# Kernel optimization log

Measured on AMD Instinct MI355X. Metric: run time of the kernel, lower is better.

## Reference

```python
import jax, jax.numpy as jnp
import numpy as np
import math

LOG2PI = math.log(2.0 * math.pi)
ALPHA, BETA, GAMMA = 1.0, 4.0, 1.0  # coefficients (mi, tc, dw_kl)


def gaussian_log_density(samples, mean, log_var):
    inv_sigma = jnp.exp(-log_var)
    tmp = samples - mean
    return -0.5 * (tmp * tmp * inv_sigma + log_var + LOG2PI)


def log_importance_weight_matrix(batch_size, dataset_size):
    # Faithful port of the TF/beta-tcvae MSS importance weights.
    N = float(dataset_size)
    M = batch_size - 1
    strat_weight = (N - M) / (N * M)
    W = jnp.full((batch_size, batch_size), 1.0 / M, dtype=jnp.float32)
    W = W.at[:, 0].set(1.0 / N)
    W = W.at[:, 1].set(strat_weight)
    W = W.at[M - 1, 0].set(strat_weight)
    return jnp.log(W)


def setup_inputs() -> dict:
    key = jax.random.key(0)
    k1, k2, k3, k4, k5 = jax.random.split(key, 5)
    B, D, F = 2048, 16, 512
    return {
        "x": jax.random.normal(k1, (B, F), dtype=jnp.float32),
        "reconstruction": jax.random.normal(k2, (B, F), dtype=jnp.float32),
        "mu": jax.random.normal(k3, (B, D), dtype=jnp.float32),
        "log_var": jax.random.normal(k4, (B, D), dtype=jnp.float32) * 0.5,
        "z": jax.random.normal(k5, (B, D), dtype=jnp.float32),
        "size_dataset": 100000,
    }


def reference(x, reconstruction, mu, log_var, z, size_dataset):
    B = z.shape[0]
    # reconstruction loss: mean over batch of per-sample MAE == global mean abs error
    recon_loss = jnp.mean(jnp.abs(x - reconstruction))

    # log q(z|x): [B]
    log_q_zx = jnp.sum(gaussian_log_density(z, mu, log_var), axis=-1)

    # pairwise densities: [B, B, D]  (z_i under q(.|x_j))
    log_qz_prob = gaussian_log_density(z[:, None, :], mu[None, :, :], log_var[None, :, :])

    # log p(z): note the original passes ones_like(z) as log_var (faithful quirk)
    log_prior = jnp.sum(
        gaussian_log_density(z, jnp.zeros_like(z), jnp.ones_like(z)), axis=-1
    )

    # MSS importance weights [B, B]
    logiw = log_importance_weight_matrix(B, size_dataset)

    # log q(z): logsumexp over batch of joint densities + weights
    log_qz = jax.nn.logsumexp(jnp.sum(log_qz_prob, axis=2) + logiw, axis=1)  # [B]

    # log prod_d q(z_d): dimension-wise logsumexp then sum over dims
    log_qz_product = jnp.sum(
        jax.nn.logsumexp(log_qz_prob + logiw[:, :, None], axis=1), axis=1
    )  # [B]

    mutual_info_loss = jnp.mean(log_q_zx - log_qz)
    tc_loss = jnp.mean(log_qz - log_qz_product)
    dimension_wise_kl = jnp.mean(log_qz_product - log_prior)

    total_loss = (
        recon_loss
        + ALPHA * mutual_info_loss
        + BETA * tc_loss
        + GAMMA * dimension_wise_kl
    )
    return total_loss
```

## Files before the change

kernel.cpp:

```cpp
#include <hip/hip_runtime.h>
#include <math.h>

#define LOG2PI_F 1.8378770664093453f
#define LOG2E_F  1.4426950408889634f
#define LN2_F    0.6931471805599453f
#define EXP_NEG1 0.36787944117144233f

#define TI   16
#define JSP  8
#define STG  64
#define ROWF 52

__device__ __forceinline__ float exp2_(float x) { return __builtin_amdgcn_exp2f(x); }
__device__ __forceinline__ float log2_(float x) { return __builtin_amdgcn_logf(x); }


__global__ __launch_bounds__(256) void k_recon(const float4* __restrict__ x,
                                               const float4* __restrict__ r,
                                               float* __restrict__ acc, int n4) {
    float s = 0.0f;
    for (int idx = blockIdx.x * 256 + threadIdx.x; idx < n4; idx += gridDim.x * 256) {
        float4 a = x[idx], b = r[idx];
        s += fabsf(a.x - b.x) + fabsf(a.y - b.y) + fabsf(a.z - b.z) + fabsf(a.w - b.w);
    }
    #pragma unroll
    for (int off = 32; off > 0; off >>= 1) s += __shfl_down(s, off);
    __shared__ float red[4];
    int lane = threadIdx.x & 63, wv = threadIdx.x >> 6;
    if (lane == 0) red[wv] = s;
    __syncthreads();
    if (threadIdx.x == 0) atomicAdd(&acc[0], red[0] + red[1] + red[2] + red[3]);
}

__global__ __launch_bounds__(256) void k_prep(const float* __restrict__ mu,
                                              const float* __restrict__ lv,
                                              const float* __restrict__ z,
                                              const int* __restrict__ nds,
                                              float* __restrict__ AC,
                                              float* __restrict__ acc, int B) {
    int idx = blockIdx.x * 256 + threadIdx.x;
    int j = idx >> 4, d = idx & 15;
    float m = mu[idx], l = lv[idx], zz = z[idx];
    float is = __expf(-l);
    float a = -0.5f * LOG2E_F * is;
    float b = -2.0f * a * m;
    float ec = fmaf(-0.5f * LOG2E_F, l + LOG2PI_F, a * m * m);

    float Nf = (float)(*nds);
    float Mf = (float)(B - 1);
    float strat = (Nf - Mf) / (Nf * Mf);
    float w = (j == 0) ? (1.0f / Nf) : ((j == 1) ? strat : (1.0f / Mf));

    float* row = AC + (size_t)j * ROWF;
    row[d] = a;
    row[16 + d] = b;
    row[32 + d] = w * exp2_(ec);
    float es = ec;
    es += __shfl_xor(es, 1); es += __shfl_xor(es, 2);
    es += __shfl_xor(es, 4); es += __shfl_xor(es, 8);
    if (d == 0) row[48] = w * exp2_(es);

    float t = zz - m;
    float ga = -0.5f * (fmaf(t * t, is, l) + LOG2PI_F);
    float gb = -0.5f * (fmaf(zz * zz, EXP_NEG1, 1.0f) + LOG2PI_F);
    #pragma unroll
    for (int off = 32; off > 0; off >>= 1) { ga += __shfl_down(ga, off); gb += __shfl_down(gb, off); }
    __shared__ float ra[4], rb[4];
    int lane = threadIdx.x & 63, wv = threadIdx.x >> 6;
    if (lane == 0) { ra[wv] = ga; rb[wv] = gb; }
    __syncthreads();
    if (threadIdx.x == 0) {
        atomicAdd(&acc[1], ra[0] + ra[1] + ra[2] + ra[3]);
        atomicAdd(&acc[2], rb[0] + rb[1] + rb[2] + rb[3]);
    }
}

#define DIM(AQ, BQ, CQ, comp, dd, SACC) \
    e = fmaf(AQ.comp, v2[dd], BQ.comp * v[dd]); SACC += e; \
    sd[dd] = fmaf(CQ.comp, exp2_(e), sd[dd]);

__global__ __launch_bounds__(256) void k_pair(const float* __restrict__ AC,
                                              const float* __restrict__ z,
                                              float* __restrict__ Racc,
                                              int B, int jch) {
    __shared__ float sbuf[2][STG * ROWF];
    __shared__ float red[4][TI][17];

    const int il = threadIdx.x & 15;
    const int jg = threadIdx.x >> 4;
    const int i  = blockIdx.x * TI + il;
    const int jbase = blockIdx.y * jch;

    float v[16], v2[16];
    {
        const float4* zp = (const float4*)(z + (size_t)i * 16);
        float4 z0 = zp[0], z1 = zp[1], z2 = zp[2], z3 = zp[3];
        v[0]=z0.x; v[1]=z0.y; v[2]=z0.z; v[3]=z0.w;
        v[4]=z1.x; v[5]=z1.y; v[6]=z1.z; v[7]=z1.w;
        v[8]=z2.x; v[9]=z2.y; v[10]=z2.z; v[11]=z2.w;
        v[12]=z3.x; v[13]=z3.y; v[14]=z3.z; v[15]=z3.w;
        #pragma unroll
        for (int d = 0; d < 16; d++) v2[d] = v[d] * v[d];
    }

    float sd[16];
    #pragma unroll
    for (int d = 0; d < 16; d++) sd[d] = 0.0f;
    float stot = 0.0f;

    auto load_stage = [&](int buf, int st) {
        const float4* g = (const float4*)(AC + (size_t)(jbase + st * STG) * ROWF);
        float4* dst = (float4*)sbuf[buf];
        #pragma unroll
        for (int k = 0; k < 4; ++k) {
            int idx = threadIdx.x + k * 256;
            if (idx < (STG * ROWF) / 4) dst[idx] = g[idx];
        }
    };

    const int nst = jch / STG;
    load_stage(0, 0);
    __syncthreads();
    for (int st = 0; st < nst; ++st) {
        if (st + 1 < nst) load_stage((st + 1) & 1, st + 1);
        const float* base = sbuf[st & 1];
        #pragma unroll
        for (int k = 0; k < 4; ++k) {
            const float* rp = base + (jg + 16 * k) * ROWF;
            const float4* r4 = (const float4*)rp;
            float4 A0 = r4[0], A1 = r4[1], A2 = r4[2], A3 = r4[3];
            float4 Bv0 = r4[4], Bv1 = r4[5], Bv2 = r4[6], Bv3 = r4[7];
            float4 Cv0 = r4[8], Cv1 = r4[9], Cv2 = r4[10], Cv3 = r4[11];
            float  P = rp[48];
            float s2a = 0.0f, s2b = 0.0f, e;
            DIM(A0, Bv0, Cv0, x, 0, s2a)  DIM(A0, Bv0, Cv0, y, 1, s2b)
            DIM(A0, Bv0, Cv0, z, 2, s2a)  DIM(A0, Bv0, Cv0, w, 3, s2b)
            DIM(A1, Bv1, Cv1, x, 4, s2a)  DIM(A1, Bv1, Cv1, y, 5, s2b)
            DIM(A1, Bv1, Cv1, z, 6, s2a)  DIM(A1, Bv1, Cv1, w, 7, s2b)
            DIM(A2, Bv2, Cv2, x, 8, s2a)  DIM(A2, Bv2, Cv2, y, 9, s2b)
            DIM(A2, Bv2, Cv2, z, 10, s2a) DIM(A2, Bv2, Cv2, w, 11, s2b)
            DIM(A3, Bv3, Cv3, x, 12, s2a) DIM(A3, Bv3, Cv3, y, 13, s2b)
            DIM(A3, Bv3, Cv3, z, 14, s2a) DIM(A3, Bv3, Cv3, w, 15, s2b)
            stot = fmaf(P, exp2_(s2a + s2b), stot);
        }
        __syncthreads();
    }

    #pragma unroll
    for (int msk = 16; msk <= 32; msk <<= 1) {
        stot += __shfl_xor(stot, msk);
        #pragma unroll
        for (int d = 0; d < 16; d++) sd[d] += __shfl_xor(sd[d], msk);
    }
    int lane = threadIdx.x & 63, wv = threadIdx.x >> 6;
    if (lane < 16) {
        red[wv][lane][0] = stot;
        #pragma unroll
        for (int d = 0; d < 16; d++) red[wv][lane][1 + d] = sd[d];
    }
    __syncthreads();
    for (int t = threadIdx.x; t < TI * 17; t += 256) {
        int il2 = t / 17, c = t % 17;
        float s = red[0][il2][c] + red[1][il2][c] + red[2][il2][c] + red[3][il2][c];
        atomicAdd(&Racc[(size_t)(blockIdx.x * TI + il2) * 17 + c], s);
    }
}

__global__ __launch_bounds__(256) void k_logs(const float* __restrict__ Racc,
                                              const float* __restrict__ AC,
                                              const float* __restrict__ z,
                                              const int* __restrict__ nds,
                                              float* __restrict__ acc, int B) {
    int i = blockIdx.x * 256 + threadIdx.x;
    const float* R = Racc + (size_t)i * 17;
    float S = R[0];
    float Sd[16];
    #pragma unroll
    for (int d = 0; d < 16; d++) Sd[d] = R[1 + d];

    if (i == B - 2) {
        const float* row0 = AC;
        const float* vv = z + (size_t)i * 16;
        float Nf = (float)(*nds);
        float Mf = (float)(B - 1);
        float strat = (Nf - Mf) / (Nf * Mf);
        float dwN = (strat - 1.0f / Nf) * Nf;
        float s2 = 0.0f;
        #pragma unroll
        for (int d = 0; d < 16; d++) {
            float vd = vv[d];
            float e = fmaf(row0[d], vd * vd, row0[16 + d] * vd);
            s2 += e;
            Sd[d] += dwN * row0[32 + d] * exp2_(e);
        }
        S += dwN * row0[48] * exp2_(s2);
    }

    float lqz = log2_(S) * LN2_F;
    float lqzp = 0.0f;
    #pragma unroll
    for (int d = 0; d < 16; d++) lqzp += log2_(Sd[d]);
    lqzp *= LN2_F;

    #pragma unroll
    for (int off = 32; off > 0; off >>= 1) {
        lqz += __shfl_down(lqz, off);
        lqzp += __shfl_down(lqzp, off);
    }
    __shared__ float ra[4], rb[4];
    int lane = threadIdx.x & 63, wv = threadIdx.x >> 6;
    if (lane == 0) { ra[wv] = lqz; rb[wv] = lqzp; }
    __syncthreads();
    if (threadIdx.x == 0) {
        atomicAdd(&acc[3], ra[0] + ra[1] + ra[2] + ra[3]);
        atomicAdd(&acc[4], rb[0] + rb[1] + rb[2] + rb[3]);
    }
}

__global__ void k_final(const float* __restrict__ acc, float* __restrict__ out,
                        float invBF, float invB) {
    out[0] = acc[0] * invBF +
             (acc[1] + 3.0f * acc[3] - 3.0f * acc[4] - acc[2]) * invB;
}

extern "C" void kernel_launch(void* const* d_in, const int* in_sizes, int n_in,
                              void* d_out, int out_size, void* d_ws, size_t ws_size,
                              hipStream_t stream) {
    const float* x   = (const float*)d_in[0];
    const float* rec = (const float*)d_in[1];
    const float* mu  = (const float*)d_in[2];
    const float* lv  = (const float*)d_in[3];
    const float* z   = (const float*)d_in[4];
    const int*   nds = (const int*)d_in[5];

    const int BD = in_sizes[2];
    const int B  = BD / 16;
    const int BF = in_sizes[0];
    const int n4 = BF / 4;

    float* acc  = (float*)d_ws;
    float* Racc = acc + 8;
    float* AC   = Racc + (size_t)B * 17;

    hipMemsetAsync(d_ws, 0, (8 + (size_t)B * 17) * sizeof(float), stream);
    k_prep <<<BD / 256, 256, 0, stream>>>(mu, lv, z, nds, AC, acc, B);
    k_recon<<<512, 256, 0, stream>>>((const float4*)x, (const float4*)rec, acc, n4);
    dim3 gp(B / TI, JSP);
    k_pair <<<gp, 256, 0, stream>>>(AC, z, Racc, B, B / JSP);
    k_logs <<<B / 256, 256, 0, stream>>>(Racc, AC, z, nds, acc, B);
    k_final<<<1, 1, 0, stream>>>(acc, (float*)d_out, 1.0f / (float)BF, 1.0f / (float)B);
}
```

Baseline: 101.3 us.

## Read pair parameters as wave-uniform loads and replace atomics with partial buffers

```diff
diff --git a/kernel.cpp b/kernel.cpp
--- a/kernel.cpp
+++ b/kernel.cpp
@@ -6,10 +6,9 @@
 #define LN2_F    0.6931471805599453f
 #define EXP_NEG1 0.36787944117144233f
 
-#define TI   16
-#define JSP  8
-#define STG  64
 #define ROWF 52
+#define JSP  32
+#define JCW  16
 
 __device__ __forceinline__ float exp2_(float x) { return __builtin_amdgcn_exp2f(x); }
 __device__ __forceinline__ float log2_(float x) { return __builtin_amdgcn_logf(x); }
@@ -17,7 +16,7 @@
 
 __global__ __launch_bounds__(256) void k_recon(const float4* __restrict__ x,
                                                const float4* __restrict__ r,
-                                               float* __restrict__ acc, int n4) {
+                                               float* __restrict__ part, int n4) {
     float s = 0.0f;
     for (int idx = blockIdx.x * 256 + threadIdx.x; idx < n4; idx += gridDim.x * 256) {
         float4 a = x[idx], b = r[idx];
@@ -29,7 +28,7 @@
     int lane = threadIdx.x & 63, wv = threadIdx.x >> 6;
     if (lane == 0) red[wv] = s;
     __syncthreads();
-    if (threadIdx.x == 0) atomicAdd(&acc[0], red[0] + red[1] + red[2] + red[3]);
+    if (threadIdx.x == 0) part[blockIdx.x] = red[0] + red[1] + red[2] + red[3];
 }
 
 __global__ __launch_bounds__(256) void k_prep(const float* __restrict__ mu,
@@ -37,7 +36,7 @@
                                               const float* __restrict__ z,
                                               const int* __restrict__ nds,
                                               float* __restrict__ AC,
-                                              float* __restrict__ acc, int B) {
+                                              float* __restrict__ part, int B) {
     int idx = blockIdx.x * 256 + threadIdx.x;
     int j = idx >> 4, d = idx & 15;
     float m = mu[idx], l = lv[idx], zz = z[idx];
@@ -70,26 +69,22 @@
     if (lane == 0) { ra[wv] = ga; rb[wv] = gb; }
     __syncthreads();
     if (threadIdx.x == 0) {
-        atomicAdd(&acc[1], ra[0] + ra[1] + ra[2] + ra[3]);
-        atomicAdd(&acc[2], rb[0] + rb[1] + rb[2] + rb[3]);
-    }
-}
-
-#define DIM(AQ, BQ, CQ, comp, dd, SACC) \
-    e = fmaf(AQ.comp, v2[dd], BQ.comp * v[dd]); SACC += e; \
+        part[blockIdx.x * 2 + 0] = ra[0] + ra[1] + ra[2] + ra[3];
+        part[blockIdx.x * 2 + 1] = rb[0] + rb[1] + rb[2] + rb[3];
+    }
+}
+
+#define DIM(AQ, BQ, CQ, comp, dd) \
+    e = fmaf(AQ.comp, v2[dd], BQ.comp * v[dd]); s2 += e; \
     sd[dd] = fmaf(CQ.comp, exp2_(e), sd[dd]);
 
 __global__ __launch_bounds__(256) void k_pair(const float* __restrict__ AC,
                                               const float* __restrict__ z,
-                                              float* __restrict__ Racc,
-                                              int B, int jch) {
-    __shared__ float sbuf[2][STG * ROWF];
-    __shared__ float red[4][TI][17];
-
-    const int il = threadIdx.x & 15;
-    const int jg = threadIdx.x >> 4;
-    const int i  = blockIdx.x * TI + il;
-    const int jbase = blockIdx.y * jch;
+                                              float* __restrict__ Racc, int B) {
+    const int lane = threadIdx.x & 63;
+    const int w    = threadIdx.x >> 6;
+    const int i    = blockIdx.x * 64 + lane;
+    const int jbase = blockIdx.y * (4 * JCW) + w * JCW;
 
     float v[16], v2[16];
     {
@@ -108,61 +103,35 @@
     for (int d = 0; d < 16; d++) sd[d] = 0.0f;
     float stot = 0.0f;
 
-    auto load_stage = [&](int buf, int st) {
-        const float4* g = (const float4*)(AC + (size_t)(jbase + st * STG) * ROWF);
-        float4* dst = (float4*)sbuf[buf];
-        #pragma unroll
-        for (int k = 0; k < 4; ++k) {
-            int idx = threadIdx.x + k * 256;
-            if (idx < (STG * ROWF) / 4) dst[idx] = g[idx];
-        }
-    };
-
-    const int nst = jch / STG;
-    load_stage(0, 0);
-    __syncthreads();
-    for (int st = 0; st < nst; ++st) {
-        if (st + 1 < nst) load_stage((st + 1) & 1, st + 1);
-        const float* base = sbuf[st & 1];
-        #pragma unroll
-        for (int k = 0; k < 4; ++k) {
-            const float* rp = base + (jg + 16 * k) * ROWF;
-            const float4* r4 = (const float4*)rp;
-            float4 A0 = r4[0], A1 = r4[1], A2 = r4[2], A3 = r4[3];
-            float4 Bv0 = r4[4], Bv1 = r4[5], Bv2 = r4[6], Bv3 = r4[7];
-            float4 Cv0 = r4[8], Cv1 = r4[9], Cv2 = r4[10], Cv3 = r4[11];
-            float  P = rp[48];
-            float s2a = 0.0f, s2b = 0.0f, e;
-            DIM(A0, Bv0, Cv0, x, 0, s2a)  DIM(A0, Bv0, Cv0, y, 1, s2b)
-            DIM(A0, Bv0, Cv0, z, 2, s2a)  DIM(A0, Bv0, Cv0, w, 3, s2b)
-            DIM(A1, Bv1, Cv1, x, 4, s2a)  DIM(A1, Bv1, Cv1, y, 5, s2b)
-            DIM(A1, Bv1, Cv1, z, 6, s2a)  DIM(A1, Bv1, Cv1, w, 7, s2b)
-            DIM(A2, Bv2, Cv2, x, 8, s2a)  DIM(A2, Bv2, Cv2, y, 9, s2b)
-            DIM(A2, Bv2, Cv2, z, 10, s2a) DIM(A2, Bv2, Cv2, w, 11, s2b)
-            DIM(A3, Bv3, Cv3, x, 12, s2a) DIM(A3, Bv3, Cv3, y, 13, s2b)
-            DIM(A3, Bv3, Cv3, z, 14, s2a) DIM(A3, Bv3, Cv3, w, 15, s2b)
-            stot = fmaf(P, exp2_(s2a + s2b), stot);
-        }
-        __syncthreads();
-    }
-
-    #pragma unroll
-    for (int msk = 16; msk <= 32; msk <<= 1) {
-        stot += __shfl_xor(stot, msk);
-        #pragma unroll
-        for (int d = 0; d < 16; d++) sd[d] += __shfl_xor(sd[d], msk);
-    }
-    int lane = threadIdx.x & 63, wv = threadIdx.x >> 6;
-    if (lane < 16) {
-        red[wv][lane][0] = stot;
-        #pragma unroll
-        for (int d = 0; d < 16; d++) red[wv][lane][1 + d] = sd[d];
-    }
-    __syncthreads();
-    for (int t = threadIdx.x; t < TI * 17; t += 256) {
-        int il2 = t / 17, c = t % 17;
-        float s = red[0][il2][c] + red[1][il2][c] + red[2][il2][c] + red[3][il2][c];
-        atomicAdd(&Racc[(size_t)(blockIdx.x * TI + il2) * 17 + c], s);
+    #pragma unroll 2
+    for (int jj = 0; jj < JCW; ++jj) {
+        const float* rp = AC + (size_t)(jbase + jj) * ROWF;
+        const float4* r4 = (const float4*)rp;
+        float4 A0 = r4[0], A1 = r4[1], A2 = r4[2], A3 = r4[3];
+        float4 Bv0 = r4[4], Bv1 = r4[5], Bv2 = r4[6], Bv3 = r4[7];
+        float4 Cv0 = r4[8], Cv1 = r4[9], Cv2 = r4[10], Cv3 = r4[11];
+        float  P = rp[48];
+        float s2 = 0.0f, e;
+        DIM(A0, Bv0, Cv0, x, 0)  DIM(A0, Bv0, Cv0, y, 1)
+        DIM(A0, Bv0, Cv0, z, 2)  DIM(A0, Bv0, Cv0, w, 3)
+        DIM(A1, Bv1, Cv1, x, 4)  DIM(A1, Bv1, Cv1, y, 5)
+        DIM(A1, Bv1, Cv1, z, 6)  DIM(A1, Bv1, Cv1, w, 7)
+        DIM(A2, Bv2, Cv2, x, 8)  DIM(A2, Bv2, Cv2, y, 9)
+        DIM(A2, Bv2, Cv2, z, 10) DIM(A2, Bv2, Cv2, w, 11)
+        DIM(A3, Bv3, Cv3, x, 12) DIM(A3, Bv3, Cv3, y, 13)
+        DIM(A3, Bv3, Cv3, z, 14) DIM(A3, Bv3, Cv3, w, 15)
+        stot = fmaf(P, exp2_(s2), stot);
+    }
+
+    __shared__ float red[4][64][19];
+    red[w][lane][0] = stot;
+    #pragma unroll
+    for (int d = 0; d < 16; d++) red[w][lane][1 + d] = sd[d];
+    __syncthreads();
+    for (int t = threadIdx.x; t < 64 * 17; t += 256) {
+        int c = t >> 6, il = t & 63;
+        float s = red[0][il][c] + red[1][il][c] + red[2][il][c] + red[3][il][c];
+        Racc[((size_t)blockIdx.y * 17 + c) * B + blockIdx.x * 64 + il] = s;
     }
 }
 
@@ -170,57 +139,97 @@
                                               const float* __restrict__ AC,
                                               const float* __restrict__ z,
                                               const int* __restrict__ nds,
-                                              float* __restrict__ acc, int B) {
-    int i = blockIdx.x * 256 + threadIdx.x;
-    const float* R = Racc + (size_t)i * 17;
-    float S = R[0];
-    float Sd[16];
-    #pragma unroll
-    for (int d = 0; d < 16; d++) Sd[d] = R[1 + d];
+                                              float* __restrict__ part, int B) {
+    const int lane = threadIdx.x & 63;
+    const int g    = threadIdx.x >> 6;
+    const int i    = blockIdx.x * 64 + lane;
+    const int c0   = (g == 0) ? 0 : 1 + 4 * g;
+    const int nc   = (g == 0) ? 5 : 4;
+
+    float sums[5];
+    #pragma unroll
+    for (int k = 0; k < 5; k++) sums[k] = 0.0f;
+    for (int s = 0; s < JSP; ++s) {
+        #pragma unroll 5
+        for (int k = 0; k < nc; ++k)
+            sums[k] += Racc[((size_t)s * 17 + c0 + k) * B + i];
+    }
 
     if (i == B - 2) {
-        const float* row0 = AC;
-        const float* vv = z + (size_t)i * 16;
+        const float* vv = z + (size_t)(B - 2) * 16;
         float Nf = (float)(*nds);
         float Mf = (float)(B - 1);
-        float strat = (Nf - Mf) / (Nf * Mf);
-        float dwN = (strat - 1.0f / Nf) * Nf;
-        float s2 = 0.0f;
-        #pragma unroll
-        for (int d = 0; d < 16; d++) {
-            float vd = vv[d];
-            float e = fmaf(row0[d], vd * vd, row0[16 + d] * vd);
-            s2 += e;
-            Sd[d] += dwN * row0[32 + d] * exp2_(e);
+        float dwN = (Nf - 2.0f * Mf) / Mf;
+        for (int k = 0; k < nc; ++k) {
+            int c = c0 + k;
+            if (c == 0) {
+                float s2 = 0.0f;
+                #pragma unroll
+                for (int d = 0; d < 16; d++) {
+                    float vd = vv[d];
+                    s2 += fmaf(AC[d], vd * vd, AC[16 + d] * vd);
+                }
+                sums[k] += dwN * AC[48] * exp2_(s2);
+            } else {
+                int d = c - 1;
+                float vd = vv[d];
+                float e = fmaf(AC[d], vd * vd, AC[16 + d] * vd);
+                sums[k] += dwN * AC[32 + d] * exp2_(e);
+            }
         }
-        S += dwN * row0[48] * exp2_(s2);
-    }
-
-    float lqz = log2_(S) * LN2_F;
-    float lqzp = 0.0f;
-    #pragma unroll
-    for (int d = 0; d < 16; d++) lqzp += log2_(Sd[d]);
-    lqzp *= LN2_F;
-
+    }
+
+    float lqz = 0.0f, lqzp = 0.0f;
+    for (int k = 0; k < nc; ++k) {
+        float lg = log2_(sums[k]) * LN2_F;
+        if (c0 + k == 0) lqz = lg; else lqzp += lg;
+    }
     #pragma unroll
     for (int off = 32; off > 0; off >>= 1) {
-        lqz += __shfl_down(lqz, off);
+        lqz  += __shfl_down(lqz, off);
         lqzp += __shfl_down(lqzp, off);
     }
     __shared__ float ra[4], rb[4];
-    int lane = threadIdx.x & 63, wv = threadIdx.x >> 6;
-    if (lane == 0) { ra[wv] = lqz; rb[wv] = lqzp; }
+    if (lane == 0) { ra[g] = lqz; rb[g] = lqzp; }
     __syncthreads();
     if (threadIdx.x == 0) {
-        atomicAdd(&acc[3], ra[0] + ra[1] + ra[2] + ra[3]);
-        atomicAdd(&acc[4], rb[0] + rb[1] + rb[2] + rb[3]);
-    }
-}
-
-__global__ void k_final(const float* __restrict__ acc, float* __restrict__ out,
-                        float invBF, float invB) {
-    out[0] = acc[0] * invBF +
-             (acc[1] + 3.0f * acc[3] - 3.0f * acc[4] - acc[2]) * invB;
+        part[blockIdx.x * 2 + 0] = ra[0] + ra[1] + ra[2] + ra[3];
+        part[blockIdx.x * 2 + 1] = rb[0] + rb[1] + rb[2] + rb[3];
+    }
+}
+
+__global__ __launch_bounds__(256) void k_final(const float* __restrict__ ws,
+                                               float* __restrict__ out,
+                                               float invBF, float invB) {
+    const float* reconPart = ws;
+    const float* prepPart  = ws + 512;
+    const float* logsPart  = ws + 768;
+    int t = threadIdx.x;
+    float rec = 0.0f, lqzx = 0.0f, lpr = 0.0f, lqz = 0.0f, lqzp = 0.0f;
+    for (int k = t; k < 512; k += 256) rec += reconPart[k];
+    if (t < 128) { lqzx = prepPart[2 * t]; lpr = prepPart[2 * t + 1]; }
+    if (t < 32)  { lqz  = logsPart[2 * t]; lqzp = logsPart[2 * t + 1]; }
+    #pragma unroll
+    for (int off = 32; off > 0; off >>= 1) {
+        rec += __shfl_down(rec, off);   lqzx += __shfl_down(lqzx, off);
+        lpr += __shfl_down(lpr, off);   lqz  += __shfl_down(lqz, off);
+        lqzp += __shfl_down(lqzp, off);
+    }
+    __shared__ float red[4][5];
+    int lane = t & 63, wv = t >> 6;
+    if (lane == 0) {
+        red[wv][0] = rec; red[wv][1] = lqzx; red[wv][2] = lpr;
+        red[wv][3] = lqz; red[wv][4] = lqzp;
+    }
+    __syncthreads();
+    if (t == 0) {
+        float R = red[0][0] + red[1][0] + red[2][0] + red[3][0];
+        float X = red[0][1] + red[1][1] + red[2][1] + red[3][1];
+        float P = red[0][2] + red[1][2] + red[2][2] + red[3][2];
+        float Q = red[0][3] + red[1][3] + red[2][3] + red[3][3];
+        float D = red[0][4] + red[1][4] + red[2][4] + red[3][4];
+        out[0] = R * invBF + (X + 3.0f * Q - 3.0f * D - P) * invB;
+    }
 }
 
 extern "C" void kernel_launch(void* const* d_in, const int* in_sizes, int n_in,
@@ -238,15 +247,17 @@
     const int BF = in_sizes[0];
     const int n4 = BF / 4;
 
-    float* acc  = (float*)d_ws;
-    float* Racc = acc + 8;
-    float* AC   = Racc + (size_t)B * 17;
-
-    hipMemsetAsync(d_ws, 0, (8 + (size_t)B * 17) * sizeof(float), stream);
-    k_prep <<<BD / 256, 256, 0, stream>>>(mu, lv, z, nds, AC, acc, B);
-    k_recon<<<512, 256, 0, stream>>>((const float4*)x, (const float4*)rec, acc, n4);
-    dim3 gp(B / TI, JSP);
-    k_pair <<<gp, 256, 0, stream>>>(AC, z, Racc, B, B / JSP);
-    k_logs <<<B / 256, 256, 0, stream>>>(Racc, AC, z, nds, acc, B);
-    k_final<<<1, 1, 0, stream>>>(acc, (float*)d_out, 1.0f / (float)BF, 1.0f / (float)B);
-}
+    float* ws        = (float*)d_ws;
+    float* reconPart = ws;
+    float* prepPart  = ws + 512;
+    float* logsPart  = ws + 768;
+    float* AC        = ws + 1024;
+    float* Racc      = AC + (size_t)B * ROWF;
+
+    k_prep <<<BD / 256, 256, 0, stream>>>(mu, lv, z, nds, AC, prepPart, B);
+    k_recon<<<512, 256, 0, stream>>>((const float4*)x, (const float4*)rec, reconPart, n4);
+    dim3 gp(B / 64, JSP);
+    k_pair <<<gp, 256, 0, stream>>>(AC, z, Racc, B);
+    k_logs <<<B / 64, 256, 0, stream>>>(Racc, AC, z, nds, logsPart, B);
+    k_final<<<1, 256, 0, stream>>>(ws, (float*)d_out, 1.0f / (float)BF, 1.0f / (float)B);
+}
```

Result: slower. 123.6 us (+22.0%).
